# Performance work log

Measured on AMD Instinct MI355X. Metric: run time of the kernel, lower is better.

Reference implementation:

```python
import jax, jax.numpy as jnp
import numpy as np

KERNEL_WIDTH = 0.05      # Gaussian KDE bandwidth (Angstrom)
B_SCAT = 5.803           # neutron scattering length of O (fm)
N_ATOMS = 1024
BOX_L = 25.0
N_BINS = 400


def _trapz(y, x):
    # trapezoidal rule along last axis; x is 1D
    dx = x[1:] - x[:-1]
    return jnp.sum((y[..., 1:] + y[..., :-1]) * 0.5 * dx, axis=-1)


def setup_inputs() -> dict:
    key = jax.random.key(0)
    k1, _ = jax.random.split(key)
    positions = jax.random.uniform(k1, (N_ATOMS, 3), dtype=jnp.float32) * BOX_L
    cell = jnp.eye(3, dtype=jnp.float32) * BOX_L
    r_bins = jnp.linspace(0.1, 10.0, N_BINS, dtype=jnp.float32)
    q_bins = jnp.linspace(0.5, 25.0, N_BINS, dtype=jnp.float32)
    return {"positions": positions, "cell": cell, "r_bins": r_bins, "q_bins": q_bins}


def reference(positions, cell, r_bins, q_bins):
    w = KERNEL_WIDTH
    b = B_SCAT
    N = positions.shape[0]

    # --- minimum-image pairwise distances, upper triangle only (self-pairs) ---
    ii, jj = np.triu_indices(N, k=1)                 # static index sets, P = N(N-1)/2
    diff = positions[jj] - positions[ii]             # (P, 3), matches points_2 - points_1
    cell_inv = jnp.linalg.inv(cell)
    frac = diff @ cell_inv                            # (P, 3) fractional coords
    frac = frac - jnp.round(frac)                     # minimum image convention
    mip = frac @ cell
    d = jnp.sqrt(jnp.sum(mip * mip, axis=-1) + 1e-10)  # (P,) observed distances

    # --- Gaussian KDE binning with window mask (mask == exact exclusion) ---
    min_bin = jnp.min(r_bins) - 3.0 * w
    max_bin = jnp.max(r_bins) + 3.0 * w
    in_win = (d > min_bin) & (d < max_bin)            # (P,)
    norm = 1.0 / (w * jnp.sqrt(2.0 * jnp.pi))
    gauss = jnp.exp(-0.5 * ((r_bins[None, :] - d[:, None]) / w) ** 2) * norm  # (P, n_r)
    summed = jnp.sum(jnp.where(in_win[:, None], gauss, 0.0), axis=0)          # (n_r,)

    vol = jnp.abs(jnp.linalg.det(cell))
    n_pairs = d.shape[0]
    g_partial = vol / n_pairs * summed / (4.0 * jnp.pi * r_bins ** 2)

    # single species: frac=1, coeff = b*b*0.01; G(r) = coeff * (g_partial - 1)
    G = (b * b * 0.01) * (g_partial - 1.0)

    # --- S(Q) = 1 + 4*pi*rho/Q * int r G(r) sin(Qr) dr ---
    rho = N / vol
    integrand = (r_bins[None, :] * G[None, :] *
                 jnp.sin(q_bins[:, None] * r_bins[None, :]) /
                 (q_bins[:, None] + 1e-10))           # (n_q, n_r)
    S = 1.0 + 4.0 * jnp.pi * rho * _trapz(integrand, r_bins)

    # --- F(Q) = Q (S(Q) - 1) ---
    F = q_bins * (S - 1.0)

    return jnp.stack([G, S, F])  # (3, n_bins)
```

## Files before the change

kernel.cpp:

```cpp
#include <hip/hip_runtime.h>
#include <math.h>

#define NBINS_MAX 512
#define NMAX      1024
constexpr float KW       = 0.05f;
constexpr float INV_KW   = 20.0f;
constexpr float GNORM    = 0.3989422804014327f * INV_KW;
constexpr float COEFF    = 0.33674809f;
constexpr float FOUR_PI  = 12.566370614359172f;

constexpr float DELTA     = 5.0e-5f;
constexpr float INV_DELTA = 20000.0f;
#define NFINE (256*1024)
constexpr float GWIN      = 9.0f * KW;

#define SENTINEL (NFINE - 1)

__global__ void __launch_bounds__(256)
pair_scatter_kernel(const float* __restrict__ pos,
                    const float* __restrict__ cell,
                    const float* __restrict__ rbins,
                    unsigned int* __restrict__ fine,
                    int N, int nbins)
{
    __shared__ float sh_px[NMAX], sh_py[NMAX], sh_pz[NMAX];
    const int t = threadIdx.x;
    for (int i = t; i < N; i += blockDim.x) {
        sh_px[i] = pos[3*i + 0];
        sh_py[i] = pos[3*i + 1];
        sh_pz[i] = pos[3*i + 2];
    }

    float cm[9];
#pragma unroll
    for (int k = 0; k < 9; ++k) cm[k] = cell[k];
    const float a00 = cm[0], a01 = cm[1], a02 = cm[2];
    const float a10 = cm[3], a11 = cm[4], a12 = cm[5];
    const float a20 = cm[6], a21 = cm[7], a22 = cm[8];
    const float det = a00*(a11*a22 - a12*a21)
                    - a01*(a10*a22 - a12*a20)
                    + a02*(a10*a21 - a11*a20);
    const float id = 1.0f / det;
    float im[9];
    im[0] = (a11*a22 - a12*a21)*id;
    im[1] = (a02*a21 - a01*a22)*id;
    im[2] = (a01*a12 - a02*a11)*id;
    im[3] = (a12*a20 - a10*a22)*id;
    im[4] = (a00*a22 - a02*a20)*id;
    im[5] = (a02*a10 - a00*a12)*id;
    im[6] = (a10*a21 - a11*a20)*id;
    im[7] = (a01*a20 - a00*a21)*id;
    im[8] = (a00*a11 - a01*a10)*id;

    const float r0   = rbins[0];
    const float rend = rbins[nbins - 1];
    const float minb = r0   - 3.0f * KW;
    const float maxb = rend + 3.0f * KW;

    __syncthreads();

    const int A    = blockIdx.x;
    const int B    = N - 1 - A;
    const int cntA = N - 1 - A;
    const int cntB = (B != A) ? A : 0;
    const int tot  = cntA + cntB;

    for (int p = t; p < tot; p += blockDim.x) {
        int i, j;
        if (p < cntA) { i = A; j = A + 1 + p; }
        else          { i = B; j = B + 1 + (p - cntA); }

        const float dx = sh_px[j] - sh_px[i];
        const float dy = sh_py[j] - sh_py[i];
        const float dz = sh_pz[j] - sh_pz[i];
        float fx = dx*im[0] + dy*im[3] + dz*im[6];
        float fy = dx*im[1] + dy*im[4] + dz*im[7];
        float fz = dx*im[2] + dy*im[5] + dz*im[8];
        fx -= rintf(fx); fy -= rintf(fy); fz -= rintf(fz);
        const float mx = fx*cm[0] + fy*cm[3] + fz*cm[6];
        const float my = fx*cm[1] + fy*cm[4] + fz*cm[7];
        const float mz = fx*cm[2] + fy*cm[5] + fz*cm[8];
        const float d  = sqrtf(mx*mx + my*my + mz*mz + 1e-10f);

        if (d > minb && d < maxb) {
            int idx = (int)(d * INV_DELTA);
            atomicAdd(&fine[idx], 1u);
        }
    }
}

__global__ void __launch_bounds__(256)
ghist_kernel(const unsigned int* __restrict__ fine,
             const float* __restrict__ cell,
             const float* __restrict__ rbins,
             float* __restrict__ Gws,
             float* __restrict__ out,
             int N, int nbins)
{
    __shared__ float sh_red[4];
    const int k = blockIdx.x;
    const int t = threadIdx.x;

    const unsigned int base = fine[SENTINEL];

    const float rk  = rbins[k];
    int flo = (int)((rk - GWIN) * INV_DELTA);
    int fhi = (int)((rk + GWIN) * INV_DELTA);
    if (flo < 0) flo = 0;
    if (fhi > NFINE - 1) fhi = NFINE - 1;

    float acc = 0.0f;
    for (int f = flo + t; f <= fhi; f += 256) {
        const unsigned int c = fine[f] - base;
        const float df = ((float)f + 0.5f) * DELTA;
        const float u  = (rk - df) * INV_KW;
        acc += (float)c * __expf(-0.5f * u * u);
    }

#pragma unroll
    for (int off = 32; off > 0; off >>= 1)
        acc += __shfl_down(acc, off, 64);
    if ((t & 63) == 0) sh_red[t >> 6] = acc;
    __syncthreads();

    if (t == 0) {
        const float summed = GNORM * (sh_red[0] + sh_red[1] + sh_red[2] + sh_red[3]);
        const float a00 = cell[0], a01 = cell[1], a02 = cell[2];
        const float a10 = cell[3], a11 = cell[4], a12 = cell[5];
        const float a20 = cell[6], a21 = cell[7], a22 = cell[8];
        const float det = a00*(a11*a22 - a12*a21)
                        - a01*(a10*a22 - a12*a20)
                        + a02*(a10*a21 - a11*a20);
        const float vol     = fabsf(det);
        const float n_pairs = 0.5f * (float)N * (float)(N - 1);
        const float pref    = vol / n_pairs;
        const float g = pref * summed / (FOUR_PI * rk * rk);
        const float G = COEFF * (g - 1.0f);
        out[k]  = G;
        Gws[k]  = G;
    }
}

__global__ void __launch_bounds__(256)
sq_kernel(const float* __restrict__ Gws,
          const float* __restrict__ cell,
          const float* __restrict__ rbins,
          const float* __restrict__ qbins,
          float* __restrict__ out,
          int N, int nbins)
{
    __shared__ float sh_G[NBINS_MAX];
    __shared__ float sh_r[NBINS_MAX];
    __shared__ float sh_red[4];
    const int qi = blockIdx.x;
    const int t  = threadIdx.x;

    for (int k = t; k < nbins; k += blockDim.x) {
        sh_G[k] = Gws[k];
        sh_r[k] = rbins[k];
    }
    __syncthreads();

    const float a00 = cell[0], a01 = cell[1], a02 = cell[2];
    const float a10 = cell[3], a11 = cell[4], a12 = cell[5];
    const float a20 = cell[6], a21 = cell[7], a22 = cell[8];
    const float det = a00*(a11*a22 - a12*a21)
                    - a01*(a10*a22 - a12*a20)
                    + a02*(a10*a21 - a11*a20);
    const float vol = fabsf(det);
    const float rho = (float)N / vol;

    const float q    = qbins[qi];
    const float qinv = 1.0f / (q + 1e-10f);
    float acc = 0.0f;
    for (int k = t; k < nbins; k += blockDim.x) {
        const float r    = sh_r[k];
        const float w_lo = (k > 0)         ? (r - sh_r[k - 1]) : 0.0f;
        const float w_hi = (k < nbins - 1) ? (sh_r[k + 1] - r) : 0.0f;
        acc += 0.5f * (w_lo + w_hi) * r * sh_G[k] * __sinf(q * r) * qinv;
    }
#pragma unroll
    for (int off = 32; off > 0; off >>= 1)
        acc += __shfl_down(acc, off, 64);
    if ((t & 63) == 0) sh_red[t >> 6] = acc;
    __syncthreads();
    if (t == 0) {
        const float S = 1.0f + FOUR_PI * rho *
                        (sh_red[0] + sh_red[1] + sh_red[2] + sh_red[3]);
        out[nbins + qi]   = S;
        out[2*nbins + qi] = q * (S - 1.0f);
    }
}

extern "C" void kernel_launch(void* const* d_in, const int* in_sizes, int n_in,
                              void* d_out, int out_size, void* d_ws, size_t ws_size,
                              hipStream_t stream)
{
    const float* pos   = (const float*)d_in[0];
    const float* cell  = (const float*)d_in[1];
    const float* rbins = (const float*)d_in[2];
    const float* qbins = (const float*)d_in[3];
    float* out = (float*)d_out;

    const int N     = in_sizes[0] / 3;
    const int nbins = in_sizes[2];
    const int nrp   = (N + 1) / 2;

    unsigned int* fine = (unsigned int*)d_ws;
    float* Gws = (float*)((char*)d_ws + (size_t)NFINE * sizeof(unsigned int));

    hipLaunchKernelGGL(pair_scatter_kernel, dim3(nrp), dim3(256), 0, stream,
                       pos, cell, rbins, fine, N, nbins);
    hipLaunchKernelGGL(ghist_kernel, dim3(nbins), dim3(256), 0, stream,
                       fine, cell, rbins, Gws, out, N, nbins);
    hipLaunchKernelGGL(sq_kernel, dim3(nbins), dim3(256), 0, stream,
                       Gws, cell, rbins, qbins, out, N, nbins);
}
```

Before: 88.99 us.

## Coarsen distance histogram and add first-order residual moment correction

Each pair's distance now goes into a 20x coarser fine histogram. A second integer atomic accumulates the pair's fixed-point offset from the bin centre. The Gaussian KDE kernel then applies a first-order Taylor correction using these residual sums. This shrinks the per-bin loop in the KDE pass from about 18000 to about 900 fine bins. In exchange it doubles the atomics per pair and raises contention on fewer bins. Position staging in shared memory is also replaced with direct global loads.

After: 89.01 us. Within noise of the previous version (+0.0%).

```diff
diff --git a/kernel.cpp b/kernel.cpp
--- a/kernel.cpp
+++ b/kernel.cpp
@@ -2,17 +2,18 @@
 #include <math.h>
 
 #define NBINS_MAX 512
-#define NMAX      1024
 constexpr float KW       = 0.05f;
 constexpr float INV_KW   = 20.0f;
 constexpr float GNORM    = 0.3989422804014327f * INV_KW;
 constexpr float COEFF    = 0.33674809f;
 constexpr float FOUR_PI  = 12.566370614359172f;
 
-constexpr float DELTA     = 5.0e-5f;
-constexpr float INV_DELTA = 20000.0f;
-#define NFINE (256*1024)
+constexpr float DELTA     = 1.0e-3f;
+constexpr float INV_DELTA = 1000.0f;
+#define NFINE 16384
 constexpr float GWIN      = 9.0f * KW;
+constexpr float RSCALE    = 4194304.0f;
+constexpr float INV_RSCALE= 1.0f / RSCALE;
 
 #define SENTINEL (NFINE - 1)
 
@@ -21,15 +22,10 @@
                     const float* __restrict__ cell,
                     const float* __restrict__ rbins,
                     unsigned int* __restrict__ fine,
+                    unsigned int* __restrict__ resid,
                     int N, int nbins)
 {
-    __shared__ float sh_px[NMAX], sh_py[NMAX], sh_pz[NMAX];
     const int t = threadIdx.x;
-    for (int i = t; i < N; i += blockDim.x) {
-        sh_px[i] = pos[3*i + 0];
-        sh_py[i] = pos[3*i + 1];
-        sh_pz[i] = pos[3*i + 2];
-    }
 
     float cm[9];
 #pragma unroll
@@ -57,22 +53,23 @@
     const float minb = r0   - 3.0f * KW;
     const float maxb = rend + 3.0f * KW;
 
-    __syncthreads();
-
     const int A    = blockIdx.x;
     const int B    = N - 1 - A;
     const int cntA = N - 1 - A;
     const int cntB = (B != A) ? A : 0;
     const int tot  = cntA + cntB;
 
+    const float Ax = pos[3*A+0], Ay = pos[3*A+1], Az = pos[3*A+2];
+    const float Bx = pos[3*B+0], By = pos[3*B+1], Bz = pos[3*B+2];
+
     for (int p = t; p < tot; p += blockDim.x) {
-        int i, j;
-        if (p < cntA) { i = A; j = A + 1 + p; }
-        else          { i = B; j = B + 1 + (p - cntA); }
-
-        const float dx = sh_px[j] - sh_px[i];
-        const float dy = sh_py[j] - sh_py[i];
-        const float dz = sh_pz[j] - sh_pz[i];
+        float ix, iy, iz; int j;
+        if (p < cntA) { ix = Ax; iy = Ay; iz = Az; j = A + 1 + p; }
+        else          { ix = Bx; iy = By; iz = Bz; j = B + 1 + (p - cntA); }
+
+        const float dx = pos[3*j + 0] - ix;
+        const float dy = pos[3*j + 1] - iy;
+        const float dz = pos[3*j + 2] - iz;
         float fx = dx*im[0] + dy*im[3] + dz*im[6];
         float fy = dx*im[1] + dy*im[4] + dz*im[7];
         float fz = dx*im[2] + dy*im[5] + dz*im[8];
@@ -83,14 +80,17 @@
         const float d  = sqrtf(mx*mx + my*my + mz*mz + 1e-10f);
 
         if (d > minb && d < maxb) {
-            int idx = (int)(d * INV_DELTA);
+            const int idx = (int)(d * INV_DELTA);
+            const float e = d - ((float)idx + 0.5f) * DELTA;
             atomicAdd(&fine[idx], 1u);
+            atomicAdd(&resid[idx], (unsigned int)(int)rintf(e * RSCALE));
         }
     }
 }
 
 __global__ void __launch_bounds__(256)
 ghist_kernel(const unsigned int* __restrict__ fine,
+             const unsigned int* __restrict__ resid,
              const float* __restrict__ cell,
              const float* __restrict__ rbins,
              float* __restrict__ Gws,
@@ -101,7 +101,8 @@
     const int k = blockIdx.x;
     const int t = threadIdx.x;
 
-    const unsigned int base = fine[SENTINEL];
+    const unsigned int base_c = fine [SENTINEL];
+    const unsigned int base_r = resid[SENTINEL];
 
     const float rk  = rbins[k];
     int flo = (int)((rk - GWIN) * INV_DELTA);
@@ -111,10 +112,11 @@
 
     float acc = 0.0f;
     for (int f = flo + t; f <= fhi; f += 256) {
-        const unsigned int c = fine[f] - base;
+        const float c  = (float)(fine[f] - base_c);
+        const float R  = (float)(int)(resid[f] - base_r) * INV_RSCALE;
         const float df = ((float)f + 0.5f) * DELTA;
         const float u  = (rk - df) * INV_KW;
-        acc += (float)c * __expf(-0.5f * u * u);
+        acc += (c + u * R * INV_KW) * __expf(-0.5f * u * u);
     }
 
 #pragma unroll
@@ -206,13 +208,14 @@
     const int nbins = in_sizes[2];
     const int nrp   = (N + 1) / 2;
 
-    unsigned int* fine = (unsigned int*)d_ws;
-    float* Gws = (float*)((char*)d_ws + (size_t)NFINE * sizeof(unsigned int));
+    unsigned int* fine  = (unsigned int*)d_ws;
+    unsigned int* resid = fine + NFINE;
+    float*        Gws   = (float*)(resid + NFINE);
 
     hipLaunchKernelGGL(pair_scatter_kernel, dim3(nrp), dim3(256), 0, stream,
-                       pos, cell, rbins, fine, N, nbins);
+                       pos, cell, rbins, fine, resid, N, nbins);
     hipLaunchKernelGGL(ghist_kernel, dim3(nbins), dim3(256), 0, stream,
-                       fine, cell, rbins, Gws, out, N, nbins);
+                       fine, resid, cell, rbins, Gws, out, N, nbins);
     hipLaunchKernelGGL(sq_kernel, dim3(nbins), dim3(256), 0, stream,
                        Gws, cell, rbins, qbins, out, N, nbins);
 }
```
